# Kernel tuning notes

Measured on AMD Instinct MI355X. Metric: run time of the kernel, lower is better.

Reference implementation:

```python
import jax, jax.numpy as jnp
import numpy as np
import math

D_MODEL = 1024
N_HEADS = 16
D_HEAD = 64
GROUP_SIZE = 2
N_GROUPS = N_HEADS // GROUP_SIZE
D_MLP = 4096
BATCH = 2
SEQ = 2048
LN_EPS = 1e-5


def setup_inputs() -> dict:
    key = jax.random.key(0)
    ks = jax.random.split(key, 12)

    def xavier(k, shape):
        # torch xavier_uniform on a 3D tensor treats dim0 as fan_in, prod(rest) as fan_out
        fan_in = shape[0]
        fan_out = int(np.prod(shape[1:]))
        bound = math.sqrt(6.0 / (fan_in + fan_out))
        return jax.random.uniform(k, shape, jnp.float32, -bound, bound)

    def linear_w(k, out_f, in_f):
        bound = 1.0 / math.sqrt(in_f)
        return jax.random.uniform(k, (out_f, in_f), jnp.float32, -bound, bound)

    return {
        "x": jax.random.normal(ks[0], (BATCH, SEQ, D_MODEL), jnp.float32),
        "ln1_w": jnp.ones((D_MODEL,), jnp.float32),
        "ln1_b": jnp.zeros((D_MODEL,), jnp.float32),
        "W_Q": xavier(ks[1], (D_MODEL, N_HEADS, D_HEAD)),
        "W_K": xavier(ks[2], (D_MODEL, N_GROUPS, D_HEAD)),
        "W_V": xavier(ks[3], (D_MODEL, N_GROUPS, D_HEAD)),
        "W_out": xavier(ks[4], (D_HEAD, N_HEADS, D_MODEL)),
        "b_out": jnp.zeros((D_MODEL,), jnp.float32),
        "ln2_w": jnp.ones((D_MODEL,), jnp.float32),
        "ln2_b": jnp.zeros((D_MODEL,), jnp.float32),
        "mlp1_w": linear_w(ks[5], D_MLP, D_MODEL),
        "mlp1_b": jax.random.uniform(ks[6], (D_MLP,), jnp.float32, -1.0 / math.sqrt(D_MODEL), 1.0 / math.sqrt(D_MODEL)),
        "mlp2_w": linear_w(ks[7], D_MODEL, D_MLP),
        "mlp2_b": jax.random.uniform(ks[8], (D_MODEL,), jnp.float32, -1.0 / math.sqrt(D_MLP), 1.0 / math.sqrt(D_MLP)),
    }


def _layernorm(x, w, b):
    mu = jnp.mean(x, axis=-1, keepdims=True)
    var = jnp.var(x, axis=-1, keepdims=True)
    return (x - mu) * jax.lax.rsqrt(var + LN_EPS) * w + b


def _gqa_attention(resid, W_Q, W_K, W_V, W_out, b_out):
    b, s, _ = resid.shape
    q = jnp.einsum("bsd,dhk->bshk", resid, W_Q)            # [b, s, n_heads, d_head]
    q = q.reshape(b, s, N_GROUPS, GROUP_SIZE, D_HEAD)      # [b, s, g, gs, k]
    k = jnp.einsum("bsd,dgk->bsgk", resid, W_K)            # [b, s, g, k]
    v = jnp.einsum("bsd,dgk->bsgk", resid, W_V)
    scores = jnp.einsum("bqgik,btgk->bgiqt", q, k) / math.sqrt(D_HEAD)  # [b, g, gs, q, t]
    causal_mask = jnp.triu(jnp.ones((s, s), dtype=bool), k=1)
    scores = jnp.where(causal_mask, jnp.float32(-1000000.0), scores)
    probs = jax.nn.softmax(scores, axis=-1)
    z = jnp.einsum("bgiqt,btgk->bqgik", probs, v)          # [b, q, g, gs, k]
    z = z.reshape(b, s, N_HEADS, D_HEAD)
    return jnp.einsum("bshk,khd->bsd", z, W_out) + b_out


def reference(x, ln1_w, ln1_b, W_Q, W_K, W_V, W_out, b_out,
              ln2_w, ln2_b, mlp1_w, mlp1_b, mlp2_w, mlp2_b):
    normed = _layernorm(x, ln1_w, ln1_b)
    attn_out = _gqa_attention(normed, W_Q, W_K, W_V, W_out, b_out)
    post_attn = x + attn_out
    h = _layernorm(post_attn, ln2_w, ln2_b)
    h = jax.nn.gelu(h @ mlp1_w.T + mlp1_b, approximate=False)  # torch nn.GELU default = exact erf
    mlp_out = h @ mlp2_w.T + mlp2_b
    return post_attn + mlp_out
```

## Files before the change

kernel.cpp:

```cpp
#include <hip/hip_runtime.h>
#include <cstdint>
#include <cstddef>

typedef __attribute__((ext_vector_type(8))) short short8;
typedef __attribute__((ext_vector_type(4))) float f32x4;
typedef unsigned short u16;

#define MFMA16(a, b, c) __builtin_amdgcn_mfma_f32_16x16x32_bf16((a), (b), (c), 0, 0, 0)
#define SCL2 0.18033688011112042f

__device__ __forceinline__ u16 f2bf(float f) {
  union { float f; unsigned u; } c; c.f = f;
  unsigned r = c.u + 0x7fffu + ((c.u >> 16) & 1u);
  return (u16)(r >> 16);
}

__device__ __forceinline__ unsigned cvtpk(float a, float b) {
  unsigned r;
  asm("v_cvt_pk_bf16_f32 %0, %1, %2" : "=v"(r) : "v"(a), "v"(b));
  return r;
}


__global__ __launch_bounds__(256) void prep_wqkv(const float* __restrict__ wq,
    const float* __restrict__ wk, const float* __restrict__ wv, u16* __restrict__ outp)
{
  __shared__ float t[32][33];
  const int tx = threadIdx.x & 31, ty = threadIdx.x >> 5;
  const int n0 = blockIdx.x * 32, d0 = blockIdx.y * 32;
  const float* src; int stride, nc;
  if (n0 < 1024)      { src = wq; stride = 1024; nc = n0; }
  else if (n0 < 1536) { src = wk; stride = 512;  nc = n0 - 1024; }
  else                { src = wv; stride = 512;  nc = n0 - 1536; }
#pragma unroll
  for (int i = 0; i < 32; i += 8)
    t[ty + i][tx] = src[(size_t)(d0 + ty + i) * stride + nc + tx];
  __syncthreads();
#pragma unroll
  for (int i = 0; i < 32; i += 8)
    outp[(size_t)(n0 + ty + i) * 1024 + d0 + tx] = f2bf(t[tx][ty + i]);
}

__global__ __launch_bounds__(256) void prep_wout(const float* __restrict__ wo, u16* __restrict__ outp)
{
  __shared__ float t[32][33];
  const int tx = threadIdx.x & 31, ty = threadIdx.x >> 5;
  const int d0 = blockIdx.x * 32, c0 = blockIdx.y * 32;
#pragma unroll
  for (int i = 0; i < 32; i += 8) {
    int c = c0 + ty + i;
    t[ty + i][tx] = wo[(size_t)(c & 63) * 16384 + (size_t)(c >> 6) * 1024 + d0 + tx];
  }
  __syncthreads();
#pragma unroll
  for (int i = 0; i < 32; i += 8)
    outp[(size_t)(d0 + ty + i) * 1024 + c0 + tx] = f2bf(t[tx][ty + i]);
}

__global__ void convert_bf16(const float4* __restrict__ in, u16* __restrict__ out, int n4) {
  int i = blockIdx.x * 256 + threadIdx.x;
  if (i >= n4) return;
  float4 v = in[i];
  ushort4 o; o.x = f2bf(v.x); o.y = f2bf(v.y); o.z = f2bf(v.z); o.w = f2bf(v.w);
  ((ushort4*)out)[i] = o;
}

__global__ __launch_bounds__(256) void vt_transpose(const u16* __restrict__ qkv, u16* __restrict__ vtp)
{
  __shared__ u16 t[32][33];
  const int tx = threadIdx.x & 31, ty = threadIdx.x >> 5;
  const int t0 = blockIdx.x * 32, k0 = blockIdx.y * 32;
  const int bg = blockIdx.z, b = bg >> 3, g = bg & 7;
#pragma unroll
  for (int i = 0; i < 32; i += 8)
    t[ty + i][tx] = qkv[(size_t)(b * 2048 + t0 + ty + i) * 2048 + 1536 + g * 64 + k0 + tx];
  __syncthreads();
#pragma unroll
  for (int i = 0; i < 32; i += 8)
    vtp[(size_t)(bg * 64 + k0 + ty + i) * 2048 + t0 + tx] = t[tx][ty + i];
}

__global__ __launch_bounds__(256) void ln_bf16(const float* __restrict__ x,
    const float* __restrict__ w, const float* __restrict__ b, u16* __restrict__ out)
{
  const int row = blockIdx.x, tid = threadIdx.x;
  const float4 v = ((const float4*)(x + (size_t)row * 1024))[tid];
  float s = v.x + v.y + v.z + v.w;
  float s2 = v.x * v.x + v.y * v.y + v.z * v.z + v.w * v.w;
#pragma unroll
  for (int m = 32; m >= 1; m >>= 1) { s += __shfl_xor(s, m); s2 += __shfl_xor(s2, m); }
  __shared__ float red[8];
  if ((tid & 63) == 0) { red[tid >> 6] = s; red[4 + (tid >> 6)] = s2; }
  __syncthreads();
  s  = red[0] + red[1] + red[2] + red[3];
  s2 = red[4] + red[5] + red[6] + red[7];
  const float mu = s * (1.f / 1024.f);
  const float inv = rsqrtf(s2 * (1.f / 1024.f) - mu * mu + 1e-5f);
  const float4 wv = ((const float4*)w)[tid];
  const float4 bv = ((const float4*)b)[tid];
  ushort4 o;
  o.x = f2bf((v.x - mu) * inv * wv.x + bv.x);
  o.y = f2bf((v.y - mu) * inv * wv.y + bv.y);
  o.z = f2bf((v.z - mu) * inv * wv.z + bv.z);
  o.w = f2bf((v.w - mu) * inv * wv.w + bv.w);
  ((ushort4*)out)[(size_t)row * 256 + tid] = o;
}

#define BM 128
#define BN 128
#define BK 32

template<int EPI>
__global__ __launch_bounds__(256, 2) void gemm_bt(
    const u16* __restrict__ A, const u16* __restrict__ Bt, void* __restrict__ Cout,
    const float* __restrict__ bias, const float* __restrict__ resid,
    int M, int N, int K)
{
  __shared__ u16 As[4][BM * BK];
  __shared__ u16 Bs[4][BN * BK];
  const int tid = threadIdx.x;
  const int w = tid >> 6, lane = tid & 63;
  const int lo = lane & 15, hi = lane >> 4;
  const int mBase = blockIdx.x * BM, nBase = blockIdx.y * BN;
  const int wr = (w >> 1) * 64, wc = (w & 1) * 64;

  const f32x4 vzero = {0.f, 0.f, 0.f, 0.f};
  f32x4 acc[4][4];
#pragma unroll
  for (int i = 0; i < 4; ++i)
#pragma unroll
    for (int j = 0; j < 4; ++j) acc[i][j] = vzero;

  const int base0 = w * 2048 + lane * 16;
  int srow[2], skb[2];
#pragma unroll
  for (int c = 0; c < 2; ++c) {
    const int off = base0 + c * 1024;
    srow[c] = off >> 6;
    skb[c] = (off & 63) >> 1;
  }

  const int NT = K >> 5;

  auto stage = [&](int kt) {
    const int slot = kt & 3;
    const int k0 = kt * BK;
#pragma unroll
    for (int c = 0; c < 2; ++c) {
      const u16* ga = A  + (size_t)(mBase + srow[c]) * K + k0 + skb[c];
      const u16* gb = Bt + (size_t)(nBase + srow[c]) * K + k0 + skb[c];
      __builtin_amdgcn_global_load_lds((const __attribute__((address_space(1))) void*)ga,
          (__attribute__((address_space(3))) void*)((char*)&As[slot][0] + w * 2048 + c * 1024), 16, 0, 0);
      __builtin_amdgcn_global_load_lds((const __attribute__((address_space(1))) void*)gb,
          (__attribute__((address_space(3))) void*)((char*)&Bs[slot][0] + w * 2048 + c * 1024), 16, 0, 0);
    }
  };

  stage(0);
  stage(1);

  for (int kt = 0; kt < NT; ++kt) {
    if (kt + 2 < NT) {
      stage(kt + 2);
      asm volatile("s_waitcnt vmcnt(8)" ::: "memory");
    } else if (kt + 1 < NT) {
      asm volatile("s_waitcnt vmcnt(4)" ::: "memory");
    } else {
      asm volatile("s_waitcnt vmcnt(0)" ::: "memory");
    }
    __builtin_amdgcn_s_barrier();
    __builtin_amdgcn_sched_barrier(0);

    const int slot = kt & 3;
    short8 af[4], bf[4];
#pragma unroll
    for (int i = 0; i < 4; ++i) {
      af[i] = *(const short8*)((const char*)&As[slot][0] + (wr + i * 16 + lo) * 64 + hi * 16);
      bf[i] = *(const short8*)((const char*)&Bs[slot][0] + (wc + i * 16 + lo) * 64 + hi * 16);
    }
    __builtin_amdgcn_s_setprio(1);
#pragma unroll
    for (int i = 0; i < 4; ++i)
#pragma unroll
      for (int j = 0; j < 4; ++j)
        acc[i][j] = MFMA16(af[i], bf[j], acc[i][j]);
    __builtin_amdgcn_s_setprio(0);
  }

#pragma unroll
  for (int i = 0; i < 4; ++i) {
#pragma unroll
    for (int j = 0; j < 4; ++j) {
#pragma unroll
      for (int r = 0; r < 4; ++r) {
        const int row = mBase + wr + i * 16 + hi * 4 + r;
        const int col = nBase + wc + j * 16 + lo;
        float v = acc[i][j][r];
        if (EPI == 1 || EPI == 2) v += bias[col];
        if (EPI == 1) v += resid[(size_t)row * N + col];
        if (EPI == 2) v = 0.5f * v * (1.f + erff(v * 0.70710678118f));
        if (EPI == 3 && col < 1024) v *= SCL2;
        if (EPI == 1) ((float*)Cout)[(size_t)row * N + col] = v;
        else          ((u16*)Cout)[(size_t)row * N + col] = f2bf(v);
      }
    }
  }
}

template<int EPI>
__global__ __launch_bounds__(512, 2) void gemm256(
    const u16* __restrict__ A, const u16* __restrict__ Bt, void* __restrict__ Cout,
    const float* __restrict__ bias, const float* __restrict__ resid,
    int M, int N, int K)
{
  __shared__ u16 lds8[2][2][2][8192];
  const int tid = threadIdx.x;
  const int lane = tid & 63, lo = lane & 15, hi = lane >> 4;
  const int wid = tid >> 6, wr = wid >> 2, wc = wid & 3;
  const int mBase = blockIdx.x * 256, nBase = blockIdx.y * 256;
  const int sw = (lo & 7) << 4;

  const f32x4 vzero = {0.f, 0.f, 0.f, 0.f};
  f32x4 acc[8][4];
#pragma unroll
  for (int i = 0; i < 8; ++i)
#pragma unroll
    for (int j = 0; j < 4; ++j) acc[i][j] = vzero;

  int srow[2], scol[2];
#pragma unroll
  for (int c = 0; c < 2; ++c) {
    const int p = c * 8192 + tid * 16;
    const int r = p >> 7, bb = p & 127;
    srow[c] = r;
    scol[c] = (bb ^ ((r & 7) << 4)) >> 1;
  }

  const int NT = K >> 6;

#pragma unroll
  for (int mat = 0; mat < 2; ++mat)
#pragma unroll
    for (int half = 0; half < 2; ++half)
#pragma unroll
      for (int c = 0; c < 2; ++c) {
        const u16* g = (mat == 0)
          ? A  + (size_t)(mBase + half * 128 + srow[c]) * K + scol[c]
          : Bt + (size_t)(nBase + half * 128 + srow[c]) * K + scol[c];
        __builtin_amdgcn_global_load_lds((const __attribute__((address_space(1))) void*)g,
            (__attribute__((address_space(3))) void*)(&lds8[0][mat][half][c * 4096 + tid * 8]), 16, 0, 0);
      }
  asm volatile("s_waitcnt vmcnt(0)" ::: "memory");
  asm volatile("s_barrier" ::: "memory");

  for (int kt = 0; kt < NT; ++kt) {
    const int cur = kt & 1;
    const char* baseA = (const char*)&lds8[cur][0][wr][0];
    const char* baseB = (const char*)&lds8[cur][1][wc >> 1][0];
    const int rBB = (wc & 1) * 64;

    short8 bfr[4][2], afr[4][2];
#pragma unroll
    for (int nf = 0; nf < 4; ++nf)
#pragma unroll
      for (int ks = 0; ks < 2; ++ks)
        bfr[nf][ks] = *(const short8*)(baseB + (rBB + nf * 16 + lo) * 128 + ((ks * 64 + hi * 16) ^ sw));
#pragma unroll
    for (int mf = 0; mf < 4; ++mf)
#pragma unroll
      for (int ks = 0; ks < 2; ++ks)
        afr[mf][ks] = *(const short8*)(baseA + ((mf * 16 + lo) * 128 + ((ks * 64 + hi * 16) ^ sw)));

    if (kt + 1 < NT) {
      const int ko = (kt + 1) * 64;
#pragma unroll
      for (int mat = 0; mat < 2; ++mat)
#pragma unroll
        for (int half = 0; half < 2; ++half)
#pragma unroll
          for (int c = 0; c < 2; ++c) {
            const u16* g = (mat == 0)
              ? A  + (size_t)(mBase + half * 128 + srow[c]) * K + ko + scol[c]
              : Bt + (size_t)(nBase + half * 128 + srow[c]) * K + ko + scol[c];
            __builtin_amdgcn_global_load_lds((const __attribute__((address_space(1))) void*)g,
                (__attribute__((address_space(3))) void*)(&lds8[cur ^ 1][mat][half][c * 4096 + tid * 8]), 16, 0, 0);
          }
    }

    __builtin_amdgcn_s_setprio(1);
#pragma unroll
    for (int mf = 0; mf < 4; ++mf)
#pragma unroll
      for (int nf = 0; nf < 4; ++nf)
#pragma unroll
        for (int ks = 0; ks < 2; ++ks)
          acc[mf][nf] = MFMA16(afr[mf][ks], bfr[nf][ks], acc[mf][nf]);
    __builtin_amdgcn_s_setprio(0);

#pragma unroll
    for (int mf = 0; mf < 4; ++mf)
#pragma unroll
      for (int ks = 0; ks < 2; ++ks)
        afr[mf][ks] = *(const short8*)(baseA + (((mf + 4) * 16 + lo) * 128 + ((ks * 64 + hi * 16) ^ sw)));

    __builtin_amdgcn_s_setprio(1);
#pragma unroll
    for (int mf = 0; mf < 4; ++mf)
#pragma unroll
      for (int nf = 0; nf < 4; ++nf)
#pragma unroll
        for (int ks = 0; ks < 2; ++ks)
          acc[mf + 4][nf] = MFMA16(afr[mf][ks], bfr[nf][ks], acc[mf + 4][nf]);
    __builtin_amdgcn_s_setprio(0);

    asm volatile("s_waitcnt vmcnt(0)" ::: "memory");
    asm volatile("s_barrier" ::: "memory");
  }

#pragma unroll
  for (int mf = 0; mf < 8; ++mf) {
#pragma unroll
    for (int nf = 0; nf < 4; ++nf) {
#pragma unroll
      for (int r = 0; r < 4; ++r) {
        const int row = mBase + wr * 128 + mf * 16 + hi * 4 + r;
        const int col = nBase + wc * 64 + nf * 16 + lo;
        float v = acc[mf][nf][r];
        if (EPI != 0) v += bias[col];
        if (EPI == 1) v += resid[(size_t)row * N + col];
        if (EPI == 2) v = 0.5f * v * (1.f + erff(v * 0.70710678118f));
        if (EPI == 1) ((float*)Cout)[(size_t)row * N + col] = v;
        else          ((u16*)Cout)[(size_t)row * N + col] = f2bf(v);
      }
    }
  }
}

__global__ __launch_bounds__(256) void attn_fwd(const u16* __restrict__ qkv,
    const u16* __restrict__ vt, u16* __restrict__ z)
{
  __shared__ u16 Ks[128 * 64];
  __shared__ u16 Vs[64 * 128];
  __shared__ u16 Pl[4][32 * 72];
  const int tid = threadIdx.x;
  const int w = tid >> 6, lane = tid & 63, lo = lane & 15, hi = lane >> 4;
  const int bxr = blockIdx.x;
  const int chunk = (bxr & 1) ? (31 - (bxr >> 1)) : (bxr >> 1);
  const int bg = blockIdx.y, b = bg >> 3, g = bg & 7;
  const int h = (g << 1) | (w & 1);
  const int q0w = chunk * 64 + (w >> 1) * 32;
  const int sw = (lo & 7) << 4;

  short8 qA[2][2];
#pragma unroll
  for (int qf = 0; qf < 2; ++qf)
#pragma unroll
    for (int half = 0; half < 2; ++half)
      qA[qf][half] = *(const short8*)(qkv +
          (size_t)(b * 2048 + q0w + qf * 16 + lo) * 2048 + h * 64 + half * 32 + hi * 8);

  const f32x4 vzero = {0.f, 0.f, 0.f, 0.f};
  f32x4 zacc[2][4];
#pragma unroll
  for (int qf = 0; qf < 2; ++qf)
#pragma unroll
    for (int kf = 0; kf < 4; ++kf) zacc[qf][kf] = vzero;
  float mrun[2] = {-1e30f, -1e30f};
  float lrun[2] = {0.f, 0.f};

  const u16* kbase = qkv + (size_t)b * 2048 * 2048 + 1024 + g * 64;
  const u16* vbase = vt + (size_t)(b * 8 + g) * 64 * 2048;

  int skrow[4], skcol[4], svrow[4], svcol[4];
#pragma unroll
  for (int c = 0; c < 4; ++c) {
    const int p = tid * 16 + c * 4096;
    const int rK = p >> 7, bbK = p & 127;
    skrow[c] = rK;
    skcol[c] = (bbK ^ ((rK & 7) << 4)) >> 1;
    const int rV = p >> 8, bbV = p & 255;
    svrow[c] = rV;
    svcol[c] = (bbV ^ ((rV & 7) << 4)) >> 1;
  }

  const int nTiles = (chunk + 2) >> 1;
  u16* pw = &Pl[w][0];

  for (int it = 0; it < nTiles; ++it) {
    const int t0 = it * 128;
    __syncthreads();
#pragma unroll
    for (int c = 0; c < 4; ++c) {
      __builtin_amdgcn_global_load_lds(
          (const __attribute__((address_space(1))) void*)(kbase + (size_t)(t0 + skrow[c]) * 2048 + skcol[c]),
          (__attribute__((address_space(3))) void*)((char*)Ks + tid * 16 + c * 4096), 16, 0, 0);
      __builtin_amdgcn_global_load_lds(
          (const __attribute__((address_space(1))) void*)(vbase + (size_t)svrow[c] * 2048 + t0 + svcol[c]),
          (__attribute__((address_space(3))) void*)((char*)Vs + tid * 16 + c * 4096), 16, 0, 0);
    }
    __syncthreads();

#pragma unroll
    for (int s = 0; s < 2; ++s) {
      const int ts = t0 + s * 64;
      if (ts > q0w + 31) break;

      const char* KsB = (const char*)Ks + s * 64 * 128;
      short8 kA[4][2];
#pragma unroll
      for (int nt = 0; nt < 4; ++nt)
#pragma unroll
        for (int half = 0; half < 2; ++half)
          kA[nt][half] = *(const short8*)(KsB + (nt * 16 + lo) * 128 + ((half * 64 + hi * 16) ^ sw));

#pragma unroll
      for (int qf = 0; qf < 2; ++qf) {
        f32x4 p[4];
#pragma unroll
        for (int nt = 0; nt < 4; ++nt) {
          f32x4 t = MFMA16(kA[nt][0], qA[qf][0], vzero);
          p[nt] = MFMA16(kA[nt][1], qA[qf][1], t);
        }
        const int qrow0 = q0w + qf * 16;
        if (ts + 63 > qrow0) {
          const int rel = qrow0 + lo - ts;
#pragma unroll
          for (int nt = 0; nt < 4; ++nt)
#pragma unroll
            for (int r = 0; r < 4; ++r)
              if (nt * 16 + hi * 4 + r > rel) p[nt][r] = -1e30f;
        }
        float ma = fmaxf(fmaxf(p[0][0], p[0][1]), p[0][2]);
        float mb = fmaxf(fmaxf(p[0][3], p[1][0]), p[1][1]);
        float mc = fmaxf(fmaxf(p[1][2], p[1][3]), p[2][0]);
        float md = fmaxf(fmaxf(p[2][1], p[2][2]), p[2][3]);
        float me = fmaxf(fmaxf(p[3][0], p[3][1]), p[3][2]);
        float mx = fmaxf(fmaxf(fmaxf(ma, mb), fmaxf(mc, md)), fmaxf(me, p[3][3]));
        mx = fmaxf(mx, __shfl_xor(mx, 16));
        mx = fmaxf(mx, __shfl_xor(mx, 32));
        const float nm = fmaxf(mrun[qf], mx);
        const float sc = exp2f(mrun[qf] - nm);
        mrun[qf] = nm;
#pragma unroll
        for (int nt = 0; nt < 4; ++nt)
#pragma unroll
          for (int r = 0; r < 4; ++r) p[nt][r] = exp2f(p[nt][r] - nm);
        float s0 = (p[0][0] + p[0][1]) + (p[0][2] + p[0][3]);
        float s1 = (p[1][0] + p[1][1]) + (p[1][2] + p[1][3]);
        float s2 = (p[2][0] + p[2][1]) + (p[2][2] + p[2][3]);
        float s3 = (p[3][0] + p[3][1]) + (p[3][2] + p[3][3]);
        float rs = (s0 + s1) + (s2 + s3);
        rs += __shfl_xor(rs, 16);
        rs += __shfl_xor(rs, 32);
        lrun[qf] = lrun[qf] * sc + rs;
#pragma unroll
        for (int kf = 0; kf < 4; ++kf)
#pragma unroll
          for (int r = 0; r < 4; ++r) zacc[qf][kf][r] *= sc;
#pragma unroll
        for (int nt = 0; nt < 4; ++nt) {
          uint2 uu;
          uu.x = cvtpk(p[nt][0], p[nt][1]);
          uu.y = cvtpk(p[nt][2], p[nt][3]);
          *(uint2*)((char*)pw + (qf * 16 + lo) * 144 + nt * 32 + hi * 8) = uu;
        }
      }
      asm volatile("s_waitcnt lgkmcnt(0)" ::: "memory");
      short8 pa[2][2];
#pragma unroll
      for (int qf = 0; qf < 2; ++qf)
#pragma unroll
        for (int tc = 0; tc < 2; ++tc)
          pa[qf][tc] = *(const short8*)((const char*)pw + (qf * 16 + lo) * 144 + tc * 64 + hi * 16);
#pragma unroll
      for (int kf = 0; kf < 4; ++kf) {
#pragma unroll
        for (int tc = 0; tc < 2; ++tc) {
          const short8 vf = *(const short8*)((const char*)Vs +
              (kf * 16 + lo) * 256 + ((s * 128 + tc * 64 + hi * 16) ^ sw));
          zacc[0][kf] = MFMA16(vf, pa[0][tc], zacc[0][kf]);
          zacc[1][kf] = MFMA16(vf, pa[1][tc], zacc[1][kf]);
        }
      }
    }
  }

  u16* zp = z + (size_t)(b * 2048 + q0w) * 1024 + h * 64;
#pragma unroll
  for (int qf = 0; qf < 2; ++qf) {
    const float inv = 1.f / lrun[qf];
#pragma unroll
    for (int kf = 0; kf < 4; ++kf) {
      uint2 o;
      o.x = cvtpk(zacc[qf][kf][0] * inv, zacc[qf][kf][1] * inv);
      o.y = cvtpk(zacc[qf][kf][2] * inv, zacc[qf][kf][3] * inv);
      *(uint2*)(zp + (size_t)(qf * 16 + lo) * 1024 + kf * 16 + hi * 4) = o;
    }
  }
}


extern "C" void kernel_launch(void* const* d_in, const int* in_sizes, int n_in,
                              void* d_out, int out_size, void* d_ws, size_t ws_size,
                              hipStream_t stream)
{
  (void)in_sizes; (void)n_in; (void)out_size; (void)ws_size;
  const float* x      = (const float*)d_in[0];
  const float* ln1_w  = (const float*)d_in[1];
  const float* ln1_b  = (const float*)d_in[2];
  const float* W_Q    = (const float*)d_in[3];
  const float* W_K    = (const float*)d_in[4];
  const float* W_V    = (const float*)d_in[5];
  const float* W_out  = (const float*)d_in[6];
  const float* b_out  = (const float*)d_in[7];
  const float* ln2_w  = (const float*)d_in[8];
  const float* ln2_b  = (const float*)d_in[9];
  const float* mlp1_w = (const float*)d_in[10];
  const float* mlp1_b = (const float*)d_in[11];
  const float* mlp2_w = (const float*)d_in[12];
  const float* mlp2_b = (const float*)d_in[13];
  float* out = (float*)d_out;

  char* ws = (char*)d_ws;
  u16*   wqkv_t = (u16*)(ws + 0);
  u16*   wout_t = (u16*)(ws + 4194304);
  u16*   w1     = (u16*)(ws + 6291456);
  u16*   w2     = (u16*)(ws + 14680064);
  u16*   normed = (u16*)(ws + 23068672);
  float* post   = (float*)(ws + 31457280);
  u16*   qkv    = (u16*)(ws + 48234496);
  u16*   vtb    = (u16*)(ws + 65011712);
  u16*   zb     = (u16*)(ws + 69206016);
  u16*   hbuf   = (u16*)(ws + 48234496);

  prep_wqkv<<<dim3(64, 32), 256, 0, stream>>>(W_Q, W_K, W_V, wqkv_t);
  prep_wout<<<dim3(32, 32), 256, 0, stream>>>(W_out, wout_t);
  convert_bf16<<<4096, 256, 0, stream>>>((const float4*)mlp1_w, w1, 1048576);
  convert_bf16<<<4096, 256, 0, stream>>>((const float4*)mlp2_w, w2, 1048576);

  ln_bf16<<<4096, 256, 0, stream>>>(x, ln1_w, ln1_b, normed);
  gemm_bt<3><<<dim3(32, 16), 256, 0, stream>>>(normed, wqkv_t, qkv, nullptr, nullptr, 4096, 2048, 1024);
  vt_transpose<<<dim3(64, 2, 16), 256, 0, stream>>>(qkv, vtb);
  attn_fwd<<<dim3(32, 16), 256, 0, stream>>>(qkv, vtb, zb);
  gemm_bt<1><<<dim3(32, 8), 256, 0, stream>>>(zb, wout_t, post, b_out, x, 4096, 1024, 1024);
  ln_bf16<<<4096, 256, 0, stream>>>(post, ln2_w, ln2_b, normed);
  gemm256<2><<<dim3(16, 16), 512, 0, stream>>>(normed, w1, hbuf, mlp1_b, nullptr, 4096, 4096, 1024);
  gemm_bt<1><<<dim3(32, 8), 256, 0, stream>>>(hbuf, w2, out, mlp2_b, post, 4096, 1024, 4096);
}
```

Baseline: 280.7 us.

## Double-buffer 64-key K/V tiles in attention to overlap loads with compute

```diff
diff --git a/kernel.cpp b/kernel.cpp
--- a/kernel.cpp
+++ b/kernel.cpp
@@ -339,8 +339,8 @@
 __global__ __launch_bounds__(256) void attn_fwd(const u16* __restrict__ qkv,
     const u16* __restrict__ vt, u16* __restrict__ z)
 {
-  __shared__ u16 Ks[128 * 64];
-  __shared__ u16 Vs[64 * 128];
+  __shared__ u16 Ks[2][64 * 64];
+  __shared__ u16 Vs[2][64 * 64];
   __shared__ u16 Pl[4][32 * 72];
   const int tid = threadIdx.x;
   const int w = tid >> 6, lane = tid & 63, lo = lane & 15, hi = lane >> 4;
@@ -371,116 +371,118 @@
   const u16* kbase = qkv + (size_t)b * 2048 * 2048 + 1024 + g * 64;
   const u16* vbase = vt + (size_t)(b * 8 + g) * 64 * 2048;
 
-  int skrow[4], skcol[4], svrow[4], svcol[4];
-#pragma unroll
-  for (int c = 0; c < 4; ++c) {
+  int srow[2], scol[2];
+#pragma unroll
+  for (int c = 0; c < 2; ++c) {
     const int p = tid * 16 + c * 4096;
-    const int rK = p >> 7, bbK = p & 127;
-    skrow[c] = rK;
-    skcol[c] = (bbK ^ ((rK & 7) << 4)) >> 1;
-    const int rV = p >> 8, bbV = p & 255;
-    svrow[c] = rV;
-    svcol[c] = (bbV ^ ((rV & 7) << 4)) >> 1;
-  }
-
-  const int nTiles = (chunk + 2) >> 1;
+    const int r = p >> 7, bb = p & 127;
+    srow[c] = r;
+    scol[c] = (bb ^ ((r & 7) << 4)) >> 1;
+  }
+
+  const int nTiles = chunk + 1;
   u16* pw = &Pl[w][0];
 
+  auto stageKV = [&](int it) {
+    const int slot = it & 1;
+    const int t0 = it * 64;
+#pragma unroll
+    for (int c = 0; c < 2; ++c) {
+      __builtin_amdgcn_global_load_lds(
+          (const __attribute__((address_space(1))) void*)(kbase + (size_t)(t0 + srow[c]) * 2048 + scol[c]),
+          (__attribute__((address_space(3))) void*)((char*)&Ks[slot][0] + tid * 16 + c * 4096), 16, 0, 0);
+      __builtin_amdgcn_global_load_lds(
+          (const __attribute__((address_space(1))) void*)(vbase + (size_t)srow[c] * 2048 + t0 + scol[c]),
+          (__attribute__((address_space(3))) void*)((char*)&Vs[slot][0] + tid * 16 + c * 4096), 16, 0, 0);
+    }
+  };
+
+  stageKV(0);
+
   for (int it = 0; it < nTiles; ++it) {
-    const int t0 = it * 128;
-    __syncthreads();
-#pragma unroll
-    for (int c = 0; c < 4; ++c) {
-      __builtin_amdgcn_global_load_lds(
-          (const __attribute__((address_space(1))) void*)(kbase + (size_t)(t0 + skrow[c]) * 2048 + skcol[c]),
-          (__attribute__((address_space(3))) void*)((char*)Ks + tid * 16 + c * 4096), 16, 0, 0);
-      __builtin_amdgcn_global_load_lds(
-          (const __attribute__((address_space(1))) void*)(vbase + (size_t)svrow[c] * 2048 + t0 + svcol[c]),
-          (__attribute__((address_space(3))) void*)((char*)Vs + tid * 16 + c * 4096), 16, 0, 0);
-    }
-    __syncthreads();
-
-#pragma unroll
-    for (int s = 0; s < 2; ++s) {
-      const int ts = t0 + s * 64;
-      if (ts > q0w + 31) break;
-
-      const char* KsB = (const char*)Ks + s * 64 * 128;
-      short8 kA[4][2];
+    asm volatile("s_waitcnt vmcnt(0)" ::: "memory");
+    __builtin_amdgcn_s_barrier();
+    __builtin_amdgcn_sched_barrier(0);
+    if (it + 1 < nTiles) stageKV(it + 1);
+
+    const int slot = it & 1;
+    const int ts = it * 64;
+    const char* KsB = (const char*)&Ks[slot][0];
+    const char* VsB = (const char*)&Vs[slot][0];
+
+    short8 kA[4][2];
+#pragma unroll
+    for (int nt = 0; nt < 4; ++nt)
+#pragma unroll
+      for (int half = 0; half < 2; ++half)
+        kA[nt][half] = *(const short8*)(KsB + (nt * 16 + lo) * 128 + ((half * 64 + hi * 16) ^ sw));
+
+#pragma unroll
+    for (int qf = 0; qf < 2; ++qf) {
+      f32x4 p[4];
+#pragma unroll
+      for (int nt = 0; nt < 4; ++nt) {
+        f32x4 t = MFMA16(kA[nt][0], qA[qf][0], vzero);
+        p[nt] = MFMA16(kA[nt][1], qA[qf][1], t);
+      }
+      const int qrow0 = q0w + qf * 16;
+      if (ts + 63 > qrow0) {
+        const int rel = qrow0 + lo - ts;
+#pragma unroll
+        for (int nt = 0; nt < 4; ++nt)
+#pragma unroll
+          for (int r = 0; r < 4; ++r)
+            if (nt * 16 + hi * 4 + r > rel) p[nt][r] = -1e30f;
+      }
+      float ma = fmaxf(fmaxf(p[0][0], p[0][1]), p[0][2]);
+      float mb = fmaxf(fmaxf(p[0][3], p[1][0]), p[1][1]);
+      float mc = fmaxf(fmaxf(p[1][2], p[1][3]), p[2][0]);
+      float md = fmaxf(fmaxf(p[2][1], p[2][2]), p[2][3]);
+      float me = fmaxf(fmaxf(p[3][0], p[3][1]), p[3][2]);
+      float mx = fmaxf(fmaxf(fmaxf(ma, mb), fmaxf(mc, md)), fmaxf(me, p[3][3]));
+      mx = fmaxf(mx, __shfl_xor(mx, 16));
+      mx = fmaxf(mx, __shfl_xor(mx, 32));
+      const float nm = fmaxf(mrun[qf], mx);
+      const float sc = exp2f(mrun[qf] - nm);
+      mrun[qf] = nm;
 #pragma unroll
       for (int nt = 0; nt < 4; ++nt)
 #pragma unroll
-        for (int half = 0; half < 2; ++half)
-          kA[nt][half] = *(const short8*)(KsB + (nt * 16 + lo) * 128 + ((half * 64 + hi * 16) ^ sw));
-
-#pragma unroll
-      for (int qf = 0; qf < 2; ++qf) {
-        f32x4 p[4];
-#pragma unroll
-        for (int nt = 0; nt < 4; ++nt) {
-          f32x4 t = MFMA16(kA[nt][0], qA[qf][0], vzero);
-          p[nt] = MFMA16(kA[nt][1], qA[qf][1], t);
-        }
-        const int qrow0 = q0w + qf * 16;
-        if (ts + 63 > qrow0) {
-          const int rel = qrow0 + lo - ts;
-#pragma unroll
-          for (int nt = 0; nt < 4; ++nt)
-#pragma unroll
-            for (int r = 0; r < 4; ++r)
-              if (nt * 16 + hi * 4 + r > rel) p[nt][r] = -1e30f;
-        }
-        float ma = fmaxf(fmaxf(p[0][0], p[0][1]), p[0][2]);
-        float mb = fmaxf(fmaxf(p[0][3], p[1][0]), p[1][1]);
-        float mc = fmaxf(fmaxf(p[1][2], p[1][3]), p[2][0]);
-        float md = fmaxf(fmaxf(p[2][1], p[2][2]), p[2][3]);
-        float me = fmaxf(fmaxf(p[3][0], p[3][1]), p[3][2]);
-        float mx = fmaxf(fmaxf(fmaxf(ma, mb), fmaxf(mc, md)), fmaxf(me, p[3][3]));
-        mx = fmaxf(mx, __shfl_xor(mx, 16));
-        mx = fmaxf(mx, __shfl_xor(mx, 32));
-        const float nm = fmaxf(mrun[qf], mx);
-        const float sc = exp2f(mrun[qf] - nm);
-        mrun[qf] = nm;
-#pragma unroll
-        for (int nt = 0; nt < 4; ++nt)
-#pragma unroll
-          for (int r = 0; r < 4; ++r) p[nt][r] = exp2f(p[nt][r] - nm);
-        float s0 = (p[0][0] + p[0][1]) + (p[0][2] + p[0][3]);
-        float s1 = (p[1][0] + p[1][1]) + (p[1][2] + p[1][3]);
-        float s2 = (p[2][0] + p[2][1]) + (p[2][2] + p[2][3]);
-        float s3 = (p[3][0] + p[3][1]) + (p[3][2] + p[3][3]);
-        float rs = (s0 + s1) + (s2 + s3);
-        rs += __shfl_xor(rs, 16);
-        rs += __shfl_xor(rs, 32);
-        lrun[qf] = lrun[qf] * sc + rs;
-#pragma unroll
-        for (int kf = 0; kf < 4; ++kf)
-#pragma unroll
-          for (int r = 0; r < 4; ++r) zacc[qf][kf][r] *= sc;
-#pragma unroll
-        for (int nt = 0; nt < 4; ++nt) {
-          uint2 uu;
-          uu.x = cvtpk(p[nt][0], p[nt][1]);
-          uu.y = cvtpk(p[nt][2], p[nt][3]);
-          *(uint2*)((char*)pw + (qf * 16 + lo) * 144 + nt * 32 + hi * 8) = uu;
-        }
-      }
-      asm volatile("s_waitcnt lgkmcnt(0)" ::: "memory");
-      short8 pa[2][2];
-#pragma unroll
-      for (int qf = 0; qf < 2; ++qf)
-#pragma unroll
-        for (int tc = 0; tc < 2; ++tc)
-          pa[qf][tc] = *(const short8*)((const char*)pw + (qf * 16 + lo) * 144 + tc * 64 + hi * 16);
-#pragma unroll
-      for (int kf = 0; kf < 4; ++kf) {
-#pragma unroll
-        for (int tc = 0; tc < 2; ++tc) {
-          const short8 vf = *(const short8*)((const char*)Vs +
-              (kf * 16 + lo) * 256 + ((s * 128 + tc * 64 + hi * 16) ^ sw));
-          zacc[0][kf] = MFMA16(vf, pa[0][tc], zacc[0][kf]);
-          zacc[1][kf] = MFMA16(vf, pa[1][tc], zacc[1][kf]);
-        }
+        for (int r = 0; r < 4; ++r) p[nt][r] = exp2f(p[nt][r] - nm);
+      float s0 = (p[0][0] + p[0][1]) + (p[0][2] + p[0][3]);
+      float s1 = (p[1][0] + p[1][1]) + (p[1][2] + p[1][3]);
+      float s2 = (p[2][0] + p[2][1]) + (p[2][2] + p[2][3]);
+      float s3 = (p[3][0] + p[3][1]) + (p[3][2] + p[3][3]);
+      float rs = (s0 + s1) + (s2 + s3);
+      rs += __shfl_xor(rs, 16);
+      rs += __shfl_xor(rs, 32);
+      lrun[qf] = lrun[qf] * sc + rs;
+#pragma unroll
+      for (int kf = 0; kf < 4; ++kf)
+#pragma unroll
+        for (int r = 0; r < 4; ++r) zacc[qf][kf][r] *= sc;
+#pragma unroll
+      for (int nt = 0; nt < 4; ++nt) {
+        uint2 uu;
+        uu.x = cvtpk(p[nt][0], p[nt][1]);
+        uu.y = cvtpk(p[nt][2], p[nt][3]);
+        *(uint2*)((char*)pw + (qf * 16 + lo) * 144 + nt * 32 + hi * 8) = uu;
+      }
+    }
+    asm volatile("s_waitcnt lgkmcnt(0)" ::: "memory");
+    short8 pa[2][2];
+#pragma unroll
+    for (int qf = 0; qf < 2; ++qf)
+#pragma unroll
+      for (int tc = 0; tc < 2; ++tc)
+        pa[qf][tc] = *(const short8*)((const char*)pw + (qf * 16 + lo) * 144 + tc * 64 + hi * 16);
+#pragma unroll
+    for (int kf = 0; kf < 4; ++kf) {
+#pragma unroll
+      for (int tc = 0; tc < 2; ++tc) {
+        const short8 vf = *(const short8*)(VsB + (kf * 16 + lo) * 128 + ((tc * 64 + hi * 16) ^ sw));
+        zacc[0][kf] = MFMA16(vf, pa[0][tc], zacc[0][kf]);
+        zacc[1][kf] = MFMA16(vf, pa[1][tc], zacc[1][kf]);
       }
     }
   }
```

After: 283.3 us. About the same (+0.9%).
